# Performance work log

Measured on AMD Instinct MI355X. Metric: run time of the kernel, lower is better.

The kernel has to match this reference:

```python
import jax, jax.numpy as jnp
import numpy as np

REF_MIC = 0
LOAD = 0.001 / np.sqrt(2.0)  # diagonal loading added to both real and imag parts


def _to_complex(x):
    # x: (N, 2, ...) real/imag stacked -> complex (N, ...)
    return x[:, 0] + 1j * x[:, 1]


def setup_inputs() -> dict:
    key = jax.random.key(0)
    k1, k2, k3 = jax.random.split(key, 3)
    N, C, T, F = 8, 16, 300, 257
    mixture = jax.random.normal(k1, (N, 2, C, T, F), dtype=jnp.float32)
    target = jax.random.normal(k2, (N, 2, C, T, F), dtype=jnp.float32)
    steering_vector = jax.random.normal(k3, (N, 2, C, F), dtype=jnp.float32)
    return {"mixture": mixture, "target": target, "steering_vector": steering_vector}


def reference(mixture, target, steering_vector):
    N, _, C, T, F = mixture.shape
    y = _to_complex(mixture)  # (N, C, T, F)
    x = _to_complex(target)   # (N, C, T, F)

    # Spatial covariance of mixture, mean over time frames (sum/T), fused einsum
    # phi[n,f] = (1/T) * sum_t y[n,:,t,f] y[n,:,t,f]^H  -> (N, F, C, C)
    phi = jnp.einsum('nctf,ndtf->nfcd', y, jnp.conj(y)) / T
    eye = jnp.eye(C, dtype=phi.dtype)
    # original adds load to BOTH real and imag diagonals (broadcast over RI dim)
    phi = phi + (LOAD + 1j * LOAD) * eye
    phi_inv = jnp.linalg.inv(phi)  # (N, F, C, C)

    # Cross covariance between mixture and reference-mic target
    A = jnp.transpose(y, (0, 3, 2, 1))            # (N, F, T, C)
    b = jnp.transpose(x[:, REF_MIC], (0, 2, 1))   # (N, F, T)
    mu_a = jnp.mean(A, axis=(0, 2), keepdims=True)  # mean over batch and time
    mu_b = jnp.mean(b, axis=(0, 2), keepdims=True)
    # mean over T of (A-mu_a)(b-mu_b)^H -> (N, F, C)
    phi_yx0 = jnp.mean((A - mu_a) * jnp.conj(b - mu_b)[..., None], axis=2)

    # MWF weights: w = phi_inv @ phi_yx0  -> (N, F, C)
    w = jnp.einsum('nfcd,nfd->nfc', phi_inv, phi_yx0)

    # Beamform: X_bf[n,t,f] = w[n,f]^H y[n,:,t,f]
    Xbf = jnp.einsum('nfc,nctf->ntf', jnp.conj(w), y)  # (N, T, F)

    # Back to real/imag stacked (N, 2, 1, T, F) matching torch output layout
    out = jnp.stack([Xbf.real, Xbf.imag], axis=1)[:, :, None]
    return out
```

## Files before the change

kernel.cpp:

```cpp
#include <hip/hip_runtime.h>

#define N_     8
#define C_     16
#define T_     300
#define F_     257
#define TF_    (T_*F_)
#define CTF_   (C_*TF_)
#define N2CTF_ (2*CTF_)

#define FT_    32
#define NFT_   9
#define TS_    5
#define SROW_  34
#define SSTG_  (SROW_*32)
#define SBUF_  (TS_*SSTG_)
#define NSLOT_ 3
#define NTILE_ 10
#define PHIC_  (NTILE_*16)

#define LOADC  7.0710678118654755e-04f

typedef float v2f __attribute__((ext_vector_type(2)));

__device__ __forceinline__ float2 cmul(float2 a, float2 b) {
  return make_float2(a.x*b.x - a.y*b.y, a.x*b.y + a.y*b.x);
}
__device__ __forceinline__ float2 cmulc(float2 a, float2 b) {
  return make_float2(a.x*b.x + a.y*b.y, a.y*b.x - a.x*b.y);
}
__device__ __forceinline__ float2 cdiv(float2 a, float2 b) {
  float inv = 1.0f / (b.x*b.x + b.y*b.y);
  return make_float2((a.x*b.x + a.y*b.y)*inv, (a.y*b.x - a.x*b.y)*inv);
}
__device__ __forceinline__ float2 cadd(float2 a, float2 b){ return make_float2(a.x+b.x, a.y+b.y); }
__device__ __forceinline__ float2 csub(float2 a, float2 b){ return make_float2(a.x-b.x, a.y-b.y); }

__device__ __forceinline__ void gload4(const float* g, float* l) {
  __builtin_amdgcn_global_load_lds(
      (const __attribute__((address_space(1))) unsigned int*)g,
      (__attribute__((address_space(3))) unsigned int*)l, 4, 0, 0);
}

template<int TCH>
__global__ __launch_bounds__(320) void k1_cov(const float* __restrict__ mix,
                                              const float* __restrict__ tgt,
                                              float2* __restrict__ phi_pf,
                                              float2* __restrict__ syx_pf,
                                              float2* __restrict__ sy_pf,
                                              float2* __restrict__ sx_pf) {
  __shared__ float ys[NSLOT_ * SBUF_];
  v2f* phi_p = (v2f*)phi_pf;
  v2f* syx_p = (v2f*)syx_pf;
  v2f* sy_p  = (v2f*)sy_pf;
  v2f* sx_p  = (v2f*)sx_pf;
  const int tid = threadIdx.x;
  const int ft = blockIdx.x, tc = blockIdx.y, n = blockIdx.z;
  const int fbase = ft * FT_;
  const int t0 = tc * TCH;
  const int fl = tid & 31;
  const int g  = tid >> 5;
  int ti = 0, tj = g;
  while (tj > ti) { ++ti; tj -= ti; }
  const int c0 = ti * 4;
  const int d0 = tj * 4;
  const bool sThread = (tj == 0);

  const int w     = tid >> 6;
  const int plane = (tid >> 5) & 1;
  const int f_ld  = min(fbase + fl, F_ - 1);

  const float* mixN = mix + n * N2CTF_;
  const float* tgtN = tgt + n * N2CTF_;
  const float* ysrc = mixN + plane * CTF_ + (t0 + w) * F_ + f_ld;
  const float* xsrc = tgtN + plane * CTF_ + (t0 + w) * F_ + f_ld;

  v2f acc[4][4];
  #pragma unroll
  for (int i = 0; i < 4; ++i)
    #pragma unroll
    for (int j = 0; j < 4; ++j) acc[i][j] = (v2f){0.f, 0.f};
  v2f syx[4], sy[4], sx = (v2f){0.f, 0.f};
  #pragma unroll
  for (int i = 0; i < 4; ++i) { syx[i] = (v2f){0.f,0.f}; sy[i] = (v2f){0.f,0.f}; }

  constexpr int NS = TCH / TS_;
  static_assert(NS >= 3, "ring needs >=3 stages");

  auto issue = [&](int stg) {
    float* dst = &ys[(stg % NSLOT_) * SBUF_ + w * SSTG_];
    const float* yp = ysrc + stg * (TS_ * F_);
    #pragma unroll
    for (int c = 0; c < 16; ++c) gload4(yp + c * TF_, dst + 2 * c * 32);
    gload4(xsrc + stg * (TS_ * F_), dst + 32 * 32);
  };

  issue(0);
  issue(1);

  for (int s = 0; s < NS; ++s) {
    if (s + 2 < NS) {
      issue(s + 2);
      asm volatile("s_waitcnt vmcnt(34)" ::: "memory");
    } else if (s + 1 < NS) {
      asm volatile("s_waitcnt vmcnt(17)" ::: "memory");
    } else {
      asm volatile("s_waitcnt vmcnt(0)" ::: "memory");
    }
    __builtin_amdgcn_sched_barrier(0);
    __builtin_amdgcn_s_barrier();

    const float* bufc = &ys[(s % NSLOT_) * SBUF_];
    #pragma unroll
    for (int tl = 0; tl < TS_; ++tl) {
      const float* rt = bufc + tl * SSTG_;
      v2f a[4], bu[4], bv[4];
      #pragma unroll
      for (int i = 0; i < 4; ++i) {
        float re = rt[(2 * (c0 + i)) * 32 + fl];
        float im = rt[(2 * (c0 + i)) * 32 + 32 + fl];
        a[i] = (v2f){re, im};
      }
      #pragma unroll
      for (int j = 0; j < 4; ++j) {
        float re = rt[(2 * (d0 + j)) * 32 + fl];
        float im = rt[(2 * (d0 + j)) * 32 + 32 + fl];
        bu[j] = (v2f){re, -im};
        bv[j] = (v2f){im,  re};
      }
      #pragma unroll
      for (int i = 0; i < 4; ++i)
        #pragma unroll
        for (int j = 0; j < 4; ++j)
          acc[i][j] += a[i].x * bu[j] + a[i].y * bv[j];
      if (sThread) {
        float xre = rt[32 * 32 + fl];
        float xim = rt[33 * 32 + fl];
        v2f xu = (v2f){xre, -xim};
        v2f xw = (v2f){xim,  xre};
        #pragma unroll
        for (int i = 0; i < 4; ++i) {
          syx[i] += a[i].x * xu + a[i].y * xw;
          sy[i]  += a[i];
        }
        if (g == 0) sx += (v2f){xre, xim};
      }
    }
    asm volatile("s_waitcnt lgkmcnt(0)" ::: "memory");
    __builtin_amdgcn_sched_barrier(0);
    __builtin_amdgcn_s_barrier();
  }

  const int f = fbase + fl;
  if (f < F_) {
    const int tcn = tc * N_ + n;
    v2f* pb = phi_p + ((size_t)tcn * F_ + f) * PHIC_ + g * 16;
    #pragma unroll
    for (int i = 0; i < 4; ++i)
      #pragma unroll
      for (int j = 0; j < 4; ++j) pb[i * 4 + j] = acc[i][j];
    if (sThread) {
      v2f* s1 = syx_p + ((size_t)tcn * F_ + f) * C_ + c0;
      v2f* s2 = sy_p  + ((size_t)tcn * F_ + f) * C_ + c0;
      #pragma unroll
      for (int i = 0; i < 4; ++i) { s1[i] = syx[i]; s2[i] = sy[i]; }
      if (g == 0) sx_p[(size_t)tcn * F_ + f] = sx;
    }
  }
}

template<int TCP>
__global__ __launch_bounds__(256) void k2_fused(const float2* __restrict__ phi_p,
                                                const float2* __restrict__ syx_p,
                                                const float2* __restrict__ sy_p,
                                                const float2* __restrict__ sx_p,
                                                float* __restrict__ wre,
                                                float* __restrict__ wim) {
  __shared__ float2 ld_sy[TCP * N_ * C_];
  __shared__ float2 ld_syx[TCP * C_];
  __shared__ float2 ld_sx[TCP * N_];
  __shared__ float2 Msh[16 * 17];
  __shared__ float2 muB_s, sxO_s;
  const int f = blockIdx.x, n = blockIdx.y;
  const int tid = threadIdx.x;
  const int i = tid >> 4, j = tid & 15;

  const int ti = i >> 2, tj = j >> 2, ci = i & 3, cj = j & 3;
  int gL, cell; bool cj_flip;
  if (ti >= tj) { gL = ti * (ti + 1) / 2 + tj; cell = ci * 4 + cj; cj_flip = false; }
  else          { gL = tj * (tj + 1) / 2 + ti; cell = cj * 4 + ci; cj_flip = true; }
  const int off = gL * 16 + cell;

  float2 s = make_float2(0.f, 0.f);
  for (int tc = 0; tc < TCP; ++tc) {
    float2 v = phi_p[((size_t)(tc * N_ + n) * F_ + f) * PHIC_ + off];
    s.x += v.x; s.y += v.y;
  }
  if (cj_flip) s.y = -s.y;
  if (i == j) { s.x += (float)T_ * LOADC; s.y += (float)T_ * LOADC; }

  for (int idx = tid; idx < TCP * N_ * C_; idx += 256) {
    int tcn = idx >> 4, c = idx & 15;
    ld_sy[idx] = sy_p[((size_t)tcn * F_ + f) * C_ + c];
  }
  for (int idx = tid; idx < TCP * C_; idx += 256) {
    int tc = idx >> 4, c = idx & 15;
    ld_syx[idx] = syx_p[((size_t)(tc * N_ + n) * F_ + f) * C_ + c];
  }
  for (int idx = tid; idx < TCP * N_; idx += 256) {
    ld_sx[idx] = sx_p[(size_t)idx * F_ + f];
  }
  __syncthreads();

  float2 muA_r = make_float2(0.f,0.f), ownY = make_float2(0.f,0.f), ownYX = make_float2(0.f,0.f);
  if (tid < 16) {
    float2 allY = make_float2(0.f,0.f);
    for (int tcn = 0; tcn < TCP * N_; ++tcn) allY = cadd(allY, ld_sy[tcn * C_ + tid]);
    for (int tc = 0; tc < TCP; ++tc) {
      ownY  = cadd(ownY,  ld_sy[(tc * N_ + n) * C_ + tid]);
      ownYX = cadd(ownYX, ld_syx[tc * C_ + tid]);
    }
    const float invNT = 1.0f / ((float)N_ * (float)T_);
    muA_r = make_float2(allY.x * invNT, allY.y * invNT);
  }
  if (tid == 16) {
    float2 own = make_float2(0.f,0.f), all = make_float2(0.f,0.f);
    for (int tc = 0; tc < TCP; ++tc)
      for (int nn = 0; nn < N_; ++nn) {
        float2 v = ld_sx[tc * N_ + nn];
        all = cadd(all, v);
        if (nn == n) own = cadd(own, v);
      }
    const float invNT = 1.0f / ((float)N_ * (float)T_);
    muB_s = make_float2(all.x * invNT, all.y * invNT);
    sxO_s = own;
  }
  __syncthreads();

  Msh[i * 17 + j] = s;
  if (tid < 16) {
    float2 r = ownYX;
    r = csub(r, cmulc(muA_r, sxO_s));
    r = csub(r, cmulc(ownY, muB_s));
    float2 t3 = cmulc(muA_r, muB_s);
    r.x += (float)T_ * t3.x; r.y += (float)T_ * t3.y;
    Msh[tid * 17 + 16] = r;
  }
  __syncthreads();

  for (int k = 0; k < 16; ++k) {
    float2 fac = cdiv(Msh[i * 17 + k], Msh[k * 17 + k]);
    __syncthreads();
    if (i != k) {
      Msh[i * 17 + j] = csub(Msh[i * 17 + j], cmul(fac, Msh[k * 17 + j]));
      if (j == 15) Msh[i * 17 + 16] = csub(Msh[i * 17 + 16], cmul(fac, Msh[k * 17 + 16]));
    }
    __syncthreads();
  }
  if (j == 0) {
    float2 wv = cdiv(Msh[i * 17 + 16], Msh[i * 17 + i]);
    wre[(n * C_ + i) * F_ + f] = wv.x;
    wim[(n * C_ + i) * F_ + f] = wv.y;
  }
}

__global__ __launch_bounds__(320) void k3_bf(const float* __restrict__ mix,
                                             const float* __restrict__ wre,
                                             const float* __restrict__ wim,
                                             float* __restrict__ out) {
  const int t0 = blockIdx.x * 2, n = blockIdx.y;
  const int f = threadIdx.x;
  if (f >= F_) return;
  const float* mixN = mix + n * N2CTF_;
  const float* wR = wre + n * C_ * F_;
  const float* wI = wim + n * C_ * F_;
  float* outN = out + n * 2 * TF_;
  float wr[16], wi[16];
  #pragma unroll
  for (int c = 0; c < 16; ++c) { wr[c] = wR[c * F_ + f]; wi[c] = wI[c * F_ + f]; }
  const float* yb = mixN + t0 * F_ + f;
  float xr0 = 0.f, xi0 = 0.f, xr1 = 0.f, xi1 = 0.f;
  #pragma unroll
  for (int c = 0; c < 16; ++c) {
    float yr0 = yb[c * TF_],      yi0 = yb[CTF_ + c * TF_];
    float yr1 = yb[c * TF_ + F_], yi1 = yb[CTF_ + c * TF_ + F_];
    xr0 += wr[c] * yr0 + wi[c] * yi0;
    xi0 += wr[c] * yi0 - wi[c] * yr0;
    xr1 += wr[c] * yr1 + wi[c] * yi1;
    xi1 += wr[c] * yi1 - wi[c] * yr1;
  }
  outN[t0 * F_ + f] = xr0;
  outN[TF_ + t0 * F_ + f] = xi0;
  outN[(t0 + 1) * F_ + f] = xr1;
  outN[TF_ + (t0 + 1) * F_ + f] = xi1;
}

template<int TCP>
static void launch_all(const float* mix, const float* tgt, float* ws, float* out,
                       hipStream_t stream) {
  constexpr int TCH = T_ / TCP;
  static_assert(TCH * TCP == T_ && TCH % TS_ == 0, "chunking");
  float2* phi_p = (float2*)ws;
  float2* syx_p = phi_p + (size_t)TCP * N_ * F_ * PHIC_;
  float2* sy_p  = syx_p + (size_t)TCP * N_ * F_ * C_;
  float2* sx_p  = sy_p  + (size_t)TCP * N_ * F_ * C_;
  float*  wre   = (float*)(sx_p + (size_t)TCP * N_ * F_);
  float*  wim   = wre + N_ * C_ * F_;
  k1_cov<TCH><<<dim3(NFT_, TCP, N_), dim3(320), 0, stream>>>(mix, tgt, phi_p, syx_p, sy_p, sx_p);
  k2_fused<TCP><<<dim3(F_, N_), dim3(256), 0, stream>>>(phi_p, syx_p, sy_p, sx_p, wre, wim);
  k3_bf<<<dim3(T_ / 2, N_), dim3(320), 0, stream>>>(mix, wre, wim, out);
}

static size_t ws_need_bytes(int tcp) {
  size_t fl2 = (size_t)tcp * N_ * F_ * (PHIC_ + 2 * C_ + 1);
  return fl2 * 8 + 2ull * N_ * C_ * F_ * 4;
}

extern "C" void kernel_launch(void* const* d_in, const int* in_sizes, int n_in,
                              void* d_out, int out_size, void* d_ws, size_t ws_size,
                              hipStream_t stream) {
  const float* mix = (const float*)d_in[0];
  const float* tgt = (const float*)d_in[1];
  float* out = (float*)d_out;
  float* ws  = (float*)d_ws;
  if (ws_size >= ws_need_bytes(6))      launch_all<6>(mix, tgt, ws, out, stream);
  else if (ws_size >= ws_need_bytes(2)) launch_all<2>(mix, tgt, ws, out, stream);
  else                                  launch_all<1>(mix, tgt, ws, out, stream);
}
```

Before: 237.2 us.

## Split time axis into more chunks and switch covariance kernel to double buffering

The covariance kernel now splits the time axis into 15 chunks instead of 6, with 4 time steps per stage. This launches many more blocks (1080 instead of 432) to fill the GPU's compute units. The three-slot LDS ring with hand-placed vmcnt waits becomes a two-slot double buffer synchronised by __syncthreads, which also shrinks LDS per block so more blocks can share a CU. The cost is more per-chunk partial covariance data written to workspace and reduced by the second kernel. One of the five waves now sits idle during loads, and the simpler barrier may stall longer than the tuned waitcnt scheme.

```diff
diff --git a/kernel.cpp b/kernel.cpp
--- a/kernel.cpp
+++ b/kernel.cpp
@@ -10,11 +10,8 @@
 
 #define FT_    32
 #define NFT_   9
-#define TS_    5
 #define SROW_  34
 #define SSTG_  (SROW_*32)
-#define SBUF_  (TS_*SSTG_)
-#define NSLOT_ 3
 #define NTILE_ 10
 #define PHIC_  (NTILE_*16)
 
@@ -41,14 +38,15 @@
       (__attribute__((address_space(3))) unsigned int*)l, 4, 0, 0);
 }
 
-template<int TCH>
+template<int TCH, int TS>
 __global__ __launch_bounds__(320) void k1_cov(const float* __restrict__ mix,
                                               const float* __restrict__ tgt,
                                               float2* __restrict__ phi_pf,
                                               float2* __restrict__ syx_pf,
                                               float2* __restrict__ sy_pf,
                                               float2* __restrict__ sx_pf) {
-  __shared__ float ys[NSLOT_ * SBUF_];
+  constexpr int SBUF = TS * SSTG_;
+  __shared__ float ys[2 * SBUF];
   v2f* phi_p = (v2f*)phi_pf;
   v2f* syx_p = (v2f*)syx_pf;
   v2f* sy_p  = (v2f*)sy_pf;
@@ -83,35 +81,27 @@
   #pragma unroll
   for (int i = 0; i < 4; ++i) { syx[i] = (v2f){0.f,0.f}; sy[i] = (v2f){0.f,0.f}; }
 
-  constexpr int NS = TCH / TS_;
-  static_assert(NS >= 3, "ring needs >=3 stages");
+  constexpr int NS = TCH / TS;
+  static_assert(NS * TS == TCH, "TCH must be a multiple of TS");
 
   auto issue = [&](int stg) {
-    float* dst = &ys[(stg % NSLOT_) * SBUF_ + w * SSTG_];
-    const float* yp = ysrc + stg * (TS_ * F_);
+    if (w < TS) {
+      float* dst = &ys[(stg & 1) * SBUF + w * SSTG_];
+      const float* yp = ysrc + stg * (TS * F_);
+      #pragma unroll
+      for (int c = 0; c < 16; ++c) gload4(yp + c * TF_, dst + 2 * c * 32);
+      gload4(xsrc + stg * (TS * F_), dst + 32 * 32);
+    }
+  };
+
+  issue(0);
+
+  for (int s = 0; s < NS; ++s) {
+    __syncthreads();
+    if (s + 1 < NS) issue(s + 1);
+    const float* bufc = &ys[(s & 1) * SBUF];
     #pragma unroll
-    for (int c = 0; c < 16; ++c) gload4(yp + c * TF_, dst + 2 * c * 32);
-    gload4(xsrc + stg * (TS_ * F_), dst + 32 * 32);
-  };
-
-  issue(0);
-  issue(1);
-
-  for (int s = 0; s < NS; ++s) {
-    if (s + 2 < NS) {
-      issue(s + 2);
-      asm volatile("s_waitcnt vmcnt(34)" ::: "memory");
-    } else if (s + 1 < NS) {
-      asm volatile("s_waitcnt vmcnt(17)" ::: "memory");
-    } else {
-      asm volatile("s_waitcnt vmcnt(0)" ::: "memory");
-    }
-    __builtin_amdgcn_sched_barrier(0);
-    __builtin_amdgcn_s_barrier();
-
-    const float* bufc = &ys[(s % NSLOT_) * SBUF_];
-    #pragma unroll
-    for (int tl = 0; tl < TS_; ++tl) {
+    for (int tl = 0; tl < TS; ++tl) {
       const float* rt = bufc + tl * SSTG_;
       v2f a[4], bu[4], bv[4];
       #pragma unroll
@@ -145,9 +135,6 @@
         if (g == 0) sx += (v2f){xre, xim};
       }
     }
-    asm volatile("s_waitcnt lgkmcnt(0)" ::: "memory");
-    __builtin_amdgcn_sched_barrier(0);
-    __builtin_amdgcn_s_barrier();
   }
 
   const int f = fbase + fl;
@@ -294,18 +281,18 @@
   outN[TF_ + (t0 + 1) * F_ + f] = xi1;
 }
 
-template<int TCP>
+template<int TCP, int TS>
 static void launch_all(const float* mix, const float* tgt, float* ws, float* out,
                        hipStream_t stream) {
   constexpr int TCH = T_ / TCP;
-  static_assert(TCH * TCP == T_ && TCH % TS_ == 0, "chunking");
+  static_assert(TCH * TCP == T_ && TCH % TS == 0, "chunking");
   float2* phi_p = (float2*)ws;
   float2* syx_p = phi_p + (size_t)TCP * N_ * F_ * PHIC_;
   float2* sy_p  = syx_p + (size_t)TCP * N_ * F_ * C_;
   float2* sx_p  = sy_p  + (size_t)TCP * N_ * F_ * C_;
   float*  wre   = (float*)(sx_p + (size_t)TCP * N_ * F_);
   float*  wim   = wre + N_ * C_ * F_;
-  k1_cov<TCH><<<dim3(NFT_, TCP, N_), dim3(320), 0, stream>>>(mix, tgt, phi_p, syx_p, sy_p, sx_p);
+  k1_cov<TCH, TS><<<dim3(NFT_, TCP, N_), dim3(320), 0, stream>>>(mix, tgt, phi_p, syx_p, sy_p, sx_p);
   k2_fused<TCP><<<dim3(F_, N_), dim3(256), 0, stream>>>(phi_p, syx_p, sy_p, sx_p, wre, wim);
   k3_bf<<<dim3(T_ / 2, N_), dim3(320), 0, stream>>>(mix, wre, wim, out);
 }
@@ -322,7 +309,8 @@
   const float* tgt = (const float*)d_in[1];
   float* out = (float*)d_out;
   float* ws  = (float*)d_ws;
-  if (ws_size >= ws_need_bytes(6))      launch_all<6>(mix, tgt, ws, out, stream);
-  else if (ws_size >= ws_need_bytes(2)) launch_all<2>(mix, tgt, ws, out, stream);
-  else                                  launch_all<1>(mix, tgt, ws, out, stream);
-}
+  if (ws_size >= ws_need_bytes(15))      launch_all<15, 4>(mix, tgt, ws, out, stream);
+  else if (ws_size >= ws_need_bytes(10)) launch_all<10, 5>(mix, tgt, ws, out, stream);
+  else if (ws_size >= ws_need_bytes(2))  launch_all<2, 5>(mix, tgt, ws, out, stream);
+  else                                   launch_all<1, 5>(mix, tgt, ws, out, stream);
+}
```

Result: slower. 420.3 us (+77.2%).

## Replace LDS ring-buffer staging with direct global loads in covariance kernel

Applied to the files above, without the earlier changes.

The covariance kernel no longer stages mixture and target tiles through a three-slot shared-memory ring filled by global_load_lds. Each thread now reads its channel rows straight from global memory, relying on cache for the reuse across threads. Tile groups are remapped so that diagonal tiles (g<4) reuse their own loaded values instead of loading a second operand. The time axis is split into 10 chunks instead of 6 to launch more blocks. This drops LDS traffic and barriers but adds redundant global/L2 loads across thread groups and a larger partial-sum workspace for the reduction kernel.

```diff
diff --git a/kernel.cpp b/kernel.cpp
--- a/kernel.cpp
+++ b/kernel.cpp
@@ -10,11 +10,6 @@
 
 #define FT_    32
 #define NFT_   9
-#define TS_    5
-#define SROW_  34
-#define SSTG_  (SROW_*32)
-#define SBUF_  (TS_*SSTG_)
-#define NSLOT_ 3
 #define NTILE_ 10
 #define PHIC_  (NTILE_*16)
 
@@ -34,12 +29,6 @@
 }
 __device__ __forceinline__ float2 cadd(float2 a, float2 b){ return make_float2(a.x+b.x, a.y+b.y); }
 __device__ __forceinline__ float2 csub(float2 a, float2 b){ return make_float2(a.x-b.x, a.y-b.y); }
-
-__device__ __forceinline__ void gload4(const float* g, float* l) {
-  __builtin_amdgcn_global_load_lds(
-      (const __attribute__((address_space(1))) unsigned int*)g,
-      (__attribute__((address_space(3))) unsigned int*)l, 4, 0, 0);
-}
 
 template<int TCH>
 __global__ __launch_bounds__(320) void k1_cov(const float* __restrict__ mix,
@@ -48,7 +37,6 @@
                                               float2* __restrict__ syx_pf,
                                               float2* __restrict__ sy_pf,
                                               float2* __restrict__ sx_pf) {
-  __shared__ float ys[NSLOT_ * SBUF_];
   v2f* phi_p = (v2f*)phi_pf;
   v2f* syx_p = (v2f*)syx_pf;
   v2f* sy_p  = (v2f*)sy_pf;
@@ -59,20 +47,27 @@
   const int t0 = tc * TCH;
   const int fl = tid & 31;
   const int g  = tid >> 5;
-  int ti = 0, tj = g;
-  while (tj > ti) { ++ti; tj -= ti; }
+
+  int ti, tj;
+  if (g < 4) { ti = g; tj = g; }
+  else {
+    int k = g - 4; ti = 1;
+    while (k >= ti) { k -= ti; ++ti; }
+    tj = k;
+  }
   const int c0 = ti * 4;
   const int d0 = tj * 4;
+  const bool DIAG = (g < 4);
   const bool sThread = (tj == 0);
 
-  const int w     = tid >> 6;
-  const int plane = (tid >> 5) & 1;
-  const int f_ld  = min(fbase + fl, F_ - 1);
-
-  const float* mixN = mix + n * N2CTF_;
-  const float* tgtN = tgt + n * N2CTF_;
-  const float* ysrc = mixN + plane * CTF_ + (t0 + w) * F_ + f_ld;
-  const float* xsrc = tgtN + plane * CTF_ + (t0 + w) * F_ + f_ld;
+  const int f_ld = min(fbase + fl, F_ - 1);
+
+  const float* yre = mix + n * N2CTF_;
+  const float* yim = yre + CTF_;
+  const float* xre = tgt + n * N2CTF_;
+  const float* xim = xre + CTF_;
+
+  const int obase = t0 * F_ + f_ld;
 
   v2f acc[4][4];
   #pragma unroll
@@ -83,77 +78,53 @@
   #pragma unroll
   for (int i = 0; i < 4; ++i) { syx[i] = (v2f){0.f,0.f}; sy[i] = (v2f){0.f,0.f}; }
 
-  constexpr int NS = TCH / TS_;
-  static_assert(NS >= 3, "ring needs >=3 stages");
-
-  auto issue = [&](int stg) {
-    float* dst = &ys[(stg % NSLOT_) * SBUF_ + w * SSTG_];
-    const float* yp = ysrc + stg * (TS_ * F_);
-    #pragma unroll
-    for (int c = 0; c < 16; ++c) gload4(yp + c * TF_, dst + 2 * c * 32);
-    gload4(xsrc + stg * (TS_ * F_), dst + 32 * 32);
-  };
-
-  issue(0);
-  issue(1);
-
-  for (int s = 0; s < NS; ++s) {
-    if (s + 2 < NS) {
-      issue(s + 2);
-      asm volatile("s_waitcnt vmcnt(34)" ::: "memory");
-    } else if (s + 1 < NS) {
-      asm volatile("s_waitcnt vmcnt(17)" ::: "memory");
+  #pragma unroll 2
+  for (int t = 0; t < TCH; ++t) {
+    const int o = obase + t * F_;
+    v2f a[4], bu[4], bv[4];
+    #pragma unroll
+    for (int i = 0; i < 4; ++i) {
+      const int ro = (c0 + i) * TF_ + o;
+      a[i] = (v2f){yre[ro], yim[ro]};
+    }
+    if (DIAG) {
+      #pragma unroll
+      for (int j = 0; j < 4; ++j) {
+        bu[j] = (v2f){a[j].x, -a[j].y};
+        bv[j] = (v2f){a[j].y,  a[j].x};
+      }
     } else {
-      asm volatile("s_waitcnt vmcnt(0)" ::: "memory");
-    }
-    __builtin_amdgcn_sched_barrier(0);
-    __builtin_amdgcn_s_barrier();
-
-    const float* bufc = &ys[(s % NSLOT_) * SBUF_];
-    #pragma unroll
-    for (int tl = 0; tl < TS_; ++tl) {
-      const float* rt = bufc + tl * SSTG_;
-      v2f a[4], bu[4], bv[4];
-      #pragma unroll
-      for (int i = 0; i < 4; ++i) {
-        float re = rt[(2 * (c0 + i)) * 32 + fl];
-        float im = rt[(2 * (c0 + i)) * 32 + 32 + fl];
-        a[i] = (v2f){re, im};
-      }
       #pragma unroll
       for (int j = 0; j < 4; ++j) {
-        float re = rt[(2 * (d0 + j)) * 32 + fl];
-        float im = rt[(2 * (d0 + j)) * 32 + 32 + fl];
+        const int ro = (d0 + j) * TF_ + o;
+        float re = yre[ro], im = yim[ro];
         bu[j] = (v2f){re, -im};
         bv[j] = (v2f){im,  re};
       }
-      #pragma unroll
-      for (int i = 0; i < 4; ++i)
-        #pragma unroll
-        for (int j = 0; j < 4; ++j)
-          acc[i][j] += a[i].x * bu[j] + a[i].y * bv[j];
-      if (sThread) {
-        float xre = rt[32 * 32 + fl];
-        float xim = rt[33 * 32 + fl];
-        v2f xu = (v2f){xre, -xim};
-        v2f xw = (v2f){xim,  xre};
-        #pragma unroll
-        for (int i = 0; i < 4; ++i) {
-          syx[i] += a[i].x * xu + a[i].y * xw;
-          sy[i]  += a[i];
-        }
-        if (g == 0) sx += (v2f){xre, xim};
-      }
-    }
-    asm volatile("s_waitcnt lgkmcnt(0)" ::: "memory");
-    __builtin_amdgcn_sched_barrier(0);
-    __builtin_amdgcn_s_barrier();
+    }
+    #pragma unroll
+    for (int i = 0; i < 4; ++i)
+      #pragma unroll
+      for (int j = 0; j < 4; ++j)
+        acc[i][j] += a[i].x * bu[j] + a[i].y * bv[j];
+    if (sThread) {
+      float xr = xre[o], xi = xim[o];
+      v2f xu = (v2f){xr, -xi};
+      v2f xw = (v2f){xi,  xr};
+      #pragma unroll
+      for (int i = 0; i < 4; ++i) {
+        syx[i] += a[i].x * xu + a[i].y * xw;
+        sy[i]  += a[i];
+      }
+      if (g == 0) sx += (v2f){xr, xi};
+    }
   }
 
   const int f = fbase + fl;
   if (f < F_) {
     const int tcn = tc * N_ + n;
-    v2f* pb = phi_p + ((size_t)tcn * F_ + f) * PHIC_ + g * 16;
+    const int gstore = ti * (ti + 1) / 2 + tj;
+    v2f* pb = phi_p + ((size_t)tcn * F_ + f) * PHIC_ + gstore * 16;
     #pragma unroll
     for (int i = 0; i < 4; ++i)
       #pragma unroll
@@ -298,7 +269,7 @@
 static void launch_all(const float* mix, const float* tgt, float* ws, float* out,
                        hipStream_t stream) {
   constexpr int TCH = T_ / TCP;
-  static_assert(TCH * TCP == T_ && TCH % TS_ == 0, "chunking");
+  static_assert(TCH * TCP == T_, "chunking");
   float2* phi_p = (float2*)ws;
   float2* syx_p = phi_p + (size_t)TCP * N_ * F_ * PHIC_;
   float2* sy_p  = syx_p + (size_t)TCP * N_ * F_ * C_;
@@ -322,7 +293,7 @@
   const float* tgt = (const float*)d_in[1];
   float* out = (float*)d_out;
   float* ws  = (float*)d_ws;
-  if (ws_size >= ws_need_bytes(6))      launch_all<6>(mix, tgt, ws, out, stream);
+  if (ws_size >= ws_need_bytes(10))     launch_all<10>(mix, tgt, ws, out, stream);
   else if (ws_size >= ws_need_bytes(2)) launch_all<2>(mix, tgt, ws, out, stream);
   else                                  launch_all<1>(mix, tgt, ws, out, stream);
 }
```

Result: slower. 269.1 us (+13.5%).

## Use double-buffered LDS staging in covariance kernel and split time twelve ways

Applied to the files above, without the earlier changes.

The three-slot ring of async global-to-LDS loads, with hand-written vmcnt waits and two barriers per stage, becomes a two-slot double buffer. Each stage has one __syncthreads, after which the next stage's loads are issued before the current one is computed. The time dimension is now split into up to 12 chunks instead of 6, so the covariance kernel launches more blocks and uses less LDS per block, which should raise occupancy. In exchange, the barrier's implicit full wait can expose load latency, and there are more partial sums to write and for the reduction kernel to combine.

```diff
diff --git a/kernel.cpp b/kernel.cpp
--- a/kernel.cpp
+++ b/kernel.cpp
@@ -14,7 +14,6 @@
 #define SROW_  34
 #define SSTG_  (SROW_*32)
 #define SBUF_  (TS_*SSTG_)
-#define NSLOT_ 3
 #define NTILE_ 10
 #define PHIC_  (NTILE_*16)
 
@@ -48,7 +47,7 @@
                                               float2* __restrict__ syx_pf,
                                               float2* __restrict__ sy_pf,
                                               float2* __restrict__ sx_pf) {
-  __shared__ float ys[NSLOT_ * SBUF_];
+  __shared__ float ys[2 * SBUF_];
   v2f* phi_p = (v2f*)phi_pf;
   v2f* syx_p = (v2f*)syx_pf;
   v2f* sy_p  = (v2f*)sy_pf;
@@ -84,32 +83,25 @@
   for (int i = 0; i < 4; ++i) { syx[i] = (v2f){0.f,0.f}; sy[i] = (v2f){0.f,0.f}; }
 
   constexpr int NS = TCH / TS_;
-  static_assert(NS >= 3, "ring needs >=3 stages");
-
-  auto issue = [&](int stg) {
-    float* dst = &ys[(stg % NSLOT_) * SBUF_ + w * SSTG_];
-    const float* yp = ysrc + stg * (TS_ * F_);
+  static_assert(NS * TS_ == TCH, "TCH must be a multiple of TS_");
+
+  {
+    float* dst = &ys[w * SSTG_];
     #pragma unroll
-    for (int c = 0; c < 16; ++c) gload4(yp + c * TF_, dst + 2 * c * 32);
-    gload4(xsrc + stg * (TS_ * F_), dst + 32 * 32);
-  };
-
-  issue(0);
-  issue(1);
+    for (int c = 0; c < 16; ++c) gload4(ysrc + c * TF_, dst + 2 * c * 32);
+    gload4(xsrc, dst + 32 * 32);
+  }
 
   for (int s = 0; s < NS; ++s) {
-    if (s + 2 < NS) {
-      issue(s + 2);
-      asm volatile("s_waitcnt vmcnt(34)" ::: "memory");
-    } else if (s + 1 < NS) {
-      asm volatile("s_waitcnt vmcnt(17)" ::: "memory");
-    } else {
-      asm volatile("s_waitcnt vmcnt(0)" ::: "memory");
-    }
-    __builtin_amdgcn_sched_barrier(0);
-    __builtin_amdgcn_s_barrier();
-
-    const float* bufc = &ys[(s % NSLOT_) * SBUF_];
+    __syncthreads();
+    if (s + 1 < NS) {
+      float* dst = &ys[((s + 1) & 1) * SBUF_ + w * SSTG_];
+      const float* yp = ysrc + (s + 1) * (TS_ * F_);
+      #pragma unroll
+      for (int c = 0; c < 16; ++c) gload4(yp + c * TF_, dst + 2 * c * 32);
+      gload4(xsrc + (s + 1) * (TS_ * F_), dst + 32 * 32);
+    }
+    const float* bufc = &ys[(s & 1) * SBUF_];
     #pragma unroll
     for (int tl = 0; tl < TS_; ++tl) {
       const float* rt = bufc + tl * SSTG_;
@@ -145,9 +137,6 @@
         if (g == 0) sx += (v2f){xre, xim};
       }
     }
-    asm volatile("s_waitcnt lgkmcnt(0)" ::: "memory");
-    __builtin_amdgcn_sched_barrier(0);
-    __builtin_amdgcn_s_barrier();
   }
 
   const int f = fbase + fl;
@@ -322,7 +311,8 @@
   const float* tgt = (const float*)d_in[1];
   float* out = (float*)d_out;
   float* ws  = (float*)d_ws;
-  if (ws_size >= ws_need_bytes(6))      launch_all<6>(mix, tgt, ws, out, stream);
-  else if (ws_size >= ws_need_bytes(2)) launch_all<2>(mix, tgt, ws, out, stream);
-  else                                  launch_all<1>(mix, tgt, ws, out, stream);
-}
+  if (ws_size >= ws_need_bytes(12))      launch_all<12>(mix, tgt, ws, out, stream);
+  else if (ws_size >= ws_need_bytes(10)) launch_all<10>(mix, tgt, ws, out, stream);
+  else if (ws_size >= ws_need_bytes(2))  launch_all<2>(mix, tgt, ws, out, stream);
+  else                                   launch_all<1>(mix, tgt, ws, out, stream);
+}
```

New measurement: 227.6 us. -4.0%, faster.
